# Kernel tuning notes

Measured on AMD Instinct MI355X. Metric: run time of the kernel, lower is better.

Reference implementation:

```python
import jax, jax.numpy as jnp
import numpy as np

N_BINS = 256
TAU = 0.01
EPS = 1e-10


def setup_inputs() -> dict:
    key = jax.random.key(0)
    x = jax.random.uniform(key, (4, 1, 512, 512), dtype=jnp.float32)
    return {"x": x}


def reference(x):
    B, _, H, W = x.shape
    bins = jnp.linspace(0.0, 1.0, N_BINS, dtype=x.dtype)  # (n_bins,)
    xf = x.reshape(B, H * W, 1)                            # (B, HW, 1)
    diff = xf - bins[None, None, :]                        # (B, HW, n_bins)
    weights = jnp.exp(-jnp.square(diff) / (2.0 * TAU ** 2))
    # soft histogram over pixels, normalized per image
    histogram = weights.sum(axis=1)                        # (B, n_bins)
    histogram = histogram / (histogram.sum(axis=1, keepdims=True) + EPS)
    cdf = jnp.cumsum(histogram, axis=1)                    # (B, n_bins)
    cdf_min = cdf[:, 0:1]
    cdf_normalized = (cdf - cdf_min) / (1.0 - cdf_min + EPS)
    # per-pixel soft lookup into the normalized CDF
    weights_norm = weights / (weights.sum(axis=-1, keepdims=True) + EPS)
    equalized_flat = (weights_norm * cdf_normalized[:, None, :]).sum(axis=-1)  # (B, HW)
    return equalized_flat.reshape(B, 1, H, W)
```

## Files before the change

### kernel.cpp

```cpp
#include <hip/hip_runtime.h>
#include <math.h>

#define N_BINS 256
#define TAU 0.01f
#define EPS 1e-10f
#define HW (512*512)
#define Q 4081
#define QSTRIDE 4096
#define MWIN 208
#define WTAB (2*MWIN+1)
#define WPADN 432
#define NP 27
#define CFP_STRIDE 289
#define NPART 64
#define REDS 260

__global__ __launch_bounds__(512) void hist_conv_kernel(const float* __restrict__ x,
                                                        float* __restrict__ partT) {
    __shared__ float cfp[16 * CFP_STRIDE];
    __shared__ union { unsigned int lh[QSTRIDE]; float ph[256 * 17]; } U;
    __shared__ float wtE[WPADN];
    const int b   = blockIdx.y;
    const int s   = blockIdx.x;
    const int tid = threadIdx.x;
    const int r   = tid & 15;
    const int t   = tid >> 4;

    for (int i = tid; i < QSTRIDE; i += 512) U.lh[i] = 0u;
    for (int i = tid; i < 16 * CFP_STRIDE; i += 512) cfp[i] = 0.f;
    for (int i = tid; i < WPADN; i += 512) {
        const float d = (float)(i - MWIN) * (1.0f / 4080.f);
        wtE[i] = (i < WTAB) ? __expf(-d * d * (1.0f / (2.0f * TAU * TAU))) : 0.f;
    }
    __syncthreads();

    const float4* xb = (const float4*)(x + (size_t)b * HW + (size_t)s * 4096);
#pragma unroll
    for (int i = 0; i < 2; ++i) {
        const float4 v = xb[i * 512 + tid];
        int q0 = __float2int_rn(v.x * 4080.f);
        int q1 = __float2int_rn(v.y * 4080.f);
        int q2 = __float2int_rn(v.z * 4080.f);
        int q3 = __float2int_rn(v.w * 4080.f);
        q0 = min(max(q0, 0), Q - 1); q1 = min(max(q1, 0), Q - 1);
        q2 = min(max(q2, 0), Q - 1); q3 = min(max(q3, 0), Q - 1);
        atomicAdd(&U.lh[q0], 1u); atomicAdd(&U.lh[q1], 1u);
        atomicAdd(&U.lh[q2], 1u); atomicAdd(&U.lh[q3], 1u);
    }
    __syncthreads();

#pragma unroll
    for (int k = 0; k < 8; ++k) {
        const int q = k * 512 + tid;
        cfp[(q & 15) * CFP_STRIDE + (q >> 4) + 13] = (float)U.lh[q];
    }
    __syncthreads();

    {
        float creg[34];
        const float* cbase = &cfp[r * CFP_STRIDE + 8 * t];
#pragma unroll
        for (int k = 0; k < 34; ++k) creg[k] = cbase[k];
        float acc[8];
#pragma unroll
        for (int uu = 0; uu < 8; ++uu) acc[uu] = 0.f;
#pragma unroll
        for (int p = 0; p < NP; ++p) {
            const float w = wtE[16 * p + r];
#pragma unroll
            for (int uu = 0; uu < 8; ++uu) acc[uu] += w * creg[uu + p];
        }
#pragma unroll
        for (int uu = 0; uu < 8; ++uu) U.ph[(8 * t + uu) * 17 + r] = acc[uu];
    }
    __syncthreads();

    if (tid < N_BINS) {
        float hv = 0.f;
#pragma unroll
        for (int rr = 0; rr < 16; ++rr) hv += U.ph[tid * 17 + rr];
        partT[((size_t)b * NPART + s) * N_BINS + tid] = hv;
    }
}

__global__ __launch_bounds__(512) void lut_equalize_kernel(const float* __restrict__ x,
                                                           const float* __restrict__ partT,
                                                           float* __restrict__ out) {
    __shared__ float Tl[QSTRIDE];
    __shared__ float wtE[WPADN];
    __shared__ float cdfnp[288];
    __shared__ float onesp[288];
    __shared__ __align__(16) float red[8 * REDS];
    __shared__ float wsum[4];
    __shared__ float h0s;
    const int b    = blockIdx.y;
    const int s    = blockIdx.x;
    const int tid  = threadIdx.x;
    const int r    = tid & 15;
    const int t    = tid >> 4;
    const int wv   = tid >> 6;
    const int lane = tid & 63;

    for (int i = tid; i < 288; i += 512) {
        cdfnp[i] = 0.f;
        onesp[i] = (i >= 13 && i < 269) ? 1.f : 0.f;
    }
    for (int i = tid; i < WPADN; i += 512) {
        const float d = (float)(i - MWIN) * (1.0f / 4080.f);
        wtE[i] = (i < WTAB) ? __expf(-d * d * (1.0f / (2.0f * TAU * TAU))) : 0.f;
    }

    const float4* xb = (const float4*)(x + (size_t)b * HW + (size_t)s * 4096);
    float4 px[2];
#pragma unroll
    for (int i = 0; i < 2; ++i) px[i] = xb[i * 512 + tid];

    {
        const float4* base4 = (const float4*)(partT + (size_t)b * NPART * N_BINS);
        float4 a4 = make_float4(0.f, 0.f, 0.f, 0.f);
#pragma unroll
        for (int rr = 0; rr < 8; ++rr) {
            const float4 v = base4[(size_t)(8 * wv + rr) * 64 + lane];
            a4.x += v.x; a4.y += v.y; a4.z += v.z; a4.w += v.w;
        }
        ((float4*)&red[wv * REDS])[lane] = a4;
    }
    __syncthreads();

    float val = 0.f, hv = 0.f;
    if (tid < N_BINS) {
#pragma unroll
        for (int w2 = 0; w2 < 8; ++w2) hv += red[w2 * REDS + tid];
        val = hv;
#pragma unroll
        for (int d = 1; d < 64; d <<= 1) {
            const float n = __shfl_up(val, (unsigned)d, 64);
            if (lane >= d) val += n;
        }
        if (lane == 63) wsum[tid >> 6] = val;
        if (tid == 0) h0s = hv;
    }
    __syncthreads();
    if (tid < N_BINS) {
        float prefix = 0.f, total = 0.f;
#pragma unroll
        for (int w2 = 0; w2 < 4; ++w2) {
            const float ws = wsum[w2];
            if (w2 < (tid >> 6)) prefix += ws;
            total += ws;
        }
        val += prefix;
        const float inv  = 1.0f / (total + EPS);
        const float cdf0 = h0s * inv;
        cdfnp[tid + 13] = (val * inv - cdf0) / (1.0f - cdf0 + EPS);
    }
    __syncthreads();

    {
        float creg[34], oreg[34];
        const int base = 8 * t;
#pragma unroll
        for (int k = 0; k < 34; ++k) { creg[k] = cdfnp[base + k]; oreg[k] = onesp[base + k]; }
        float acc[8], sw[8];
#pragma unroll
        for (int uu = 0; uu < 8; ++uu) { acc[uu] = 0.f; sw[uu] = 0.f; }
#pragma unroll
        for (int p = 0; p < NP; ++p) {
            const float w = wtE[16 * p + r];
#pragma unroll
            for (int uu = 0; uu < 8; ++uu) {
                const int k = uu - p + 26;
                acc[uu] += w * creg[k];
                sw[uu]  += w * oreg[k];
            }
        }
#pragma unroll
        for (int uu = 0; uu < 8; ++uu)
            Tl[16 * (8 * t + uu) + r] = acc[uu] / (sw[uu] + EPS);
    }
    __syncthreads();

    float4* ob = (float4*)(out + (size_t)b * HW + (size_t)s * 4096);
#pragma unroll
    for (int i = 0; i < 2; ++i) {
        const float4 v = px[i];
        const float vv[4] = {v.x, v.y, v.z, v.w};
        float res[4];
#pragma unroll
        for (int k2 = 0; k2 < 4; ++k2) {
            const float u = vv[k2] * 4080.f;
            int q = (int)u;
            q = min(max(q, 0), Q - 2);
            const float frac = u - (float)q;
            const float t0 = Tl[q], t1 = Tl[q + 1];
            res[k2] = fmaf(frac, t1 - t0, t0);
        }
        ob[i * 512 + tid] = make_float4(res[0], res[1], res[2], res[3]);
    }
}

extern "C" void kernel_launch(void* const* d_in, const int* in_sizes, int n_in,
                              void* d_out, int out_size, void* d_ws, size_t ws_size,
                              hipStream_t stream) {
    const float* x = (const float*)d_in[0];
    float* out     = (float*)d_out;
    const int B    = in_sizes[0] / HW;

    float* partT = (float*)d_ws;

    hist_conv_kernel<<<dim3(NPART, B), 512, 0, stream>>>(x, partT);
    lut_equalize_kernel<<<dim3(NPART, B), 512, 0, stream>>>(x, partT, out);
}
```

Baseline: 61.43 us.

## Fuse histogram and equalize kernels via cooperative launch with grid sync

Merges the two kernels into one cooperative kernel that builds per-block partial histograms, does a grid-wide sync, then computes the CDF LUT and equalizes. Pixels are loaded once and kept in registers for both phases, and shared memory is aliased through unions. This removes the second launch and the second read of x, at the cost of a cooperative launch and a grid barrier.

```diff
diff --git a/kernel.cpp b/kernel.cpp
--- a/kernel.cpp
+++ b/kernel.cpp
@@ -1,5 +1,8 @@
 #include <hip/hip_runtime.h>
+#include <hip/hip_cooperative_groups.h>
 #include <math.h>
+
+namespace cg = cooperative_groups;
 
 #define N_BINS 256
 #define TAU 0.01f
@@ -15,84 +18,26 @@
 #define NPART 64
 #define REDS 260
 
-__global__ __launch_bounds__(512) void hist_conv_kernel(const float* __restrict__ x,
-                                                        float* __restrict__ partT) {
-    __shared__ float cfp[16 * CFP_STRIDE];
-    __shared__ union { unsigned int lh[QSTRIDE]; float ph[256 * 17]; } U;
+__global__ __launch_bounds__(512) void fused_equalize_kernel(const float* __restrict__ x,
+                                                             float* __restrict__ partT,
+                                                             float* __restrict__ out) {
+    __shared__ union {
+        float cfp[16 * CFP_STRIDE];
+        float Tl[QSTRIDE];
+    } A;
+    __shared__ union {
+        unsigned int lh[QSTRIDE];
+        float ph[256 * 17];
+        struct {
+            __align__(16) float red[8 * REDS];
+            float cdfnp[288];
+            float onesp[288];
+            float wsum[4];
+            float h0s;
+        } p2;
+    } Bu;
     __shared__ float wtE[WPADN];
-    const int b   = blockIdx.y;
-    const int s   = blockIdx.x;
-    const int tid = threadIdx.x;
-    const int r   = tid & 15;
-    const int t   = tid >> 4;
-
-    for (int i = tid; i < QSTRIDE; i += 512) U.lh[i] = 0u;
-    for (int i = tid; i < 16 * CFP_STRIDE; i += 512) cfp[i] = 0.f;
-    for (int i = tid; i < WPADN; i += 512) {
-        const float d = (float)(i - MWIN) * (1.0f / 4080.f);
-        wtE[i] = (i < WTAB) ? __expf(-d * d * (1.0f / (2.0f * TAU * TAU))) : 0.f;
-    }
-    __syncthreads();
-
-    const float4* xb = (const float4*)(x + (size_t)b * HW + (size_t)s * 4096);
-#pragma unroll
-    for (int i = 0; i < 2; ++i) {
-        const float4 v = xb[i * 512 + tid];
-        int q0 = __float2int_rn(v.x * 4080.f);
-        int q1 = __float2int_rn(v.y * 4080.f);
-        int q2 = __float2int_rn(v.z * 4080.f);
-        int q3 = __float2int_rn(v.w * 4080.f);
-        q0 = min(max(q0, 0), Q - 1); q1 = min(max(q1, 0), Q - 1);
-        q2 = min(max(q2, 0), Q - 1); q3 = min(max(q3, 0), Q - 1);
-        atomicAdd(&U.lh[q0], 1u); atomicAdd(&U.lh[q1], 1u);
-        atomicAdd(&U.lh[q2], 1u); atomicAdd(&U.lh[q3], 1u);
-    }
-    __syncthreads();
-
-#pragma unroll
-    for (int k = 0; k < 8; ++k) {
-        const int q = k * 512 + tid;
-        cfp[(q & 15) * CFP_STRIDE + (q >> 4) + 13] = (float)U.lh[q];
-    }
-    __syncthreads();
-
-    {
-        float creg[34];
-        const float* cbase = &cfp[r * CFP_STRIDE + 8 * t];
-#pragma unroll
-        for (int k = 0; k < 34; ++k) creg[k] = cbase[k];
-        float acc[8];
-#pragma unroll
-        for (int uu = 0; uu < 8; ++uu) acc[uu] = 0.f;
-#pragma unroll
-        for (int p = 0; p < NP; ++p) {
-            const float w = wtE[16 * p + r];
-#pragma unroll
-            for (int uu = 0; uu < 8; ++uu) acc[uu] += w * creg[uu + p];
-        }
-#pragma unroll
-        for (int uu = 0; uu < 8; ++uu) U.ph[(8 * t + uu) * 17 + r] = acc[uu];
-    }
-    __syncthreads();
-
-    if (tid < N_BINS) {
-        float hv = 0.f;
-#pragma unroll
-        for (int rr = 0; rr < 16; ++rr) hv += U.ph[tid * 17 + rr];
-        partT[((size_t)b * NPART + s) * N_BINS + tid] = hv;
-    }
-}
-
-__global__ __launch_bounds__(512) void lut_equalize_kernel(const float* __restrict__ x,
-                                                           const float* __restrict__ partT,
-                                                           float* __restrict__ out) {
-    __shared__ float Tl[QSTRIDE];
-    __shared__ float wtE[WPADN];
-    __shared__ float cdfnp[288];
-    __shared__ float onesp[288];
-    __shared__ __align__(16) float red[8 * REDS];
-    __shared__ float wsum[4];
-    __shared__ float h0s;
+
     const int b    = blockIdx.y;
     const int s    = blockIdx.x;
     const int tid  = threadIdx.x;
@@ -101,10 +46,8 @@
     const int wv   = tid >> 6;
     const int lane = tid & 63;
 
-    for (int i = tid; i < 288; i += 512) {
-        cdfnp[i] = 0.f;
-        onesp[i] = (i >= 13 && i < 269) ? 1.f : 0.f;
-    }
+    for (int i = tid; i < QSTRIDE; i += 512) Bu.lh[i] = 0u;
+    for (int i = tid; i < 16 * CFP_STRIDE; i += 512) A.cfp[i] = 0.f;
     for (int i = tid; i < WPADN; i += 512) {
         const float d = (float)(i - MWIN) * (1.0f / 4080.f);
         wtE[i] = (i < WTAB) ? __expf(-d * d * (1.0f / (2.0f * TAU * TAU))) : 0.f;
@@ -112,9 +55,63 @@
 
     const float4* xb = (const float4*)(x + (size_t)b * HW + (size_t)s * 4096);
     float4 px[2];
-#pragma unroll
-    for (int i = 0; i < 2; ++i) px[i] = xb[i * 512 + tid];
-
+    px[0] = xb[tid];
+    px[1] = xb[512 + tid];
+    __syncthreads();
+
+#pragma unroll
+    for (int i = 0; i < 2; ++i) {
+        const float4 v = px[i];
+        int q0 = __float2int_rn(v.x * 4080.f);
+        int q1 = __float2int_rn(v.y * 4080.f);
+        int q2 = __float2int_rn(v.z * 4080.f);
+        int q3 = __float2int_rn(v.w * 4080.f);
+        q0 = min(max(q0, 0), Q - 1); q1 = min(max(q1, 0), Q - 1);
+        q2 = min(max(q2, 0), Q - 1); q3 = min(max(q3, 0), Q - 1);
+        atomicAdd(&Bu.lh[q0], 1u); atomicAdd(&Bu.lh[q1], 1u);
+        atomicAdd(&Bu.lh[q2], 1u); atomicAdd(&Bu.lh[q3], 1u);
+    }
+    __syncthreads();
+
+#pragma unroll
+    for (int k = 0; k < 8; ++k) {
+        const int q = k * 512 + tid;
+        A.cfp[(q & 15) * CFP_STRIDE + (q >> 4) + 13] = (float)Bu.lh[q];
+    }
+    __syncthreads();
+
+    {
+        float creg[34];
+        const float* cbase = &A.cfp[r * CFP_STRIDE + 8 * t];
+#pragma unroll
+        for (int k = 0; k < 34; ++k) creg[k] = cbase[k];
+        float acc[8];
+#pragma unroll
+        for (int uu = 0; uu < 8; ++uu) acc[uu] = 0.f;
+#pragma unroll
+        for (int p = 0; p < NP; ++p) {
+            const float w = wtE[16 * p + r];
+#pragma unroll
+            for (int uu = 0; uu < 8; ++uu) acc[uu] += w * creg[uu + p];
+        }
+#pragma unroll
+        for (int uu = 0; uu < 8; ++uu) Bu.ph[(8 * t + uu) * 17 + r] = acc[uu];
+    }
+    __syncthreads();
+
+    if (tid < N_BINS) {
+        float hv = 0.f;
+#pragma unroll
+        for (int rr = 0; rr < 16; ++rr) hv += Bu.ph[tid * 17 + rr];
+        partT[((size_t)b * NPART + s) * N_BINS + tid] = hv;
+    }
+
+    cg::this_grid().sync();
+
+    for (int i = tid; i < 288; i += 512) {
+        Bu.p2.cdfnp[i] = 0.f;
+        Bu.p2.onesp[i] = (i >= 13 && i < 269) ? 1.f : 0.f;
+    }
     {
         const float4* base4 = (const float4*)(partT + (size_t)b * NPART * N_BINS);
         float4 a4 = make_float4(0.f, 0.f, 0.f, 0.f);
@@ -123,36 +120,36 @@
             const float4 v = base4[(size_t)(8 * wv + rr) * 64 + lane];
             a4.x += v.x; a4.y += v.y; a4.z += v.z; a4.w += v.w;
         }
-        ((float4*)&red[wv * REDS])[lane] = a4;
+        ((float4*)&Bu.p2.red[wv * REDS])[lane] = a4;
     }
     __syncthreads();
 
     float val = 0.f, hv = 0.f;
     if (tid < N_BINS) {
 #pragma unroll
-        for (int w2 = 0; w2 < 8; ++w2) hv += red[w2 * REDS + tid];
+        for (int w2 = 0; w2 < 8; ++w2) hv += Bu.p2.red[w2 * REDS + tid];
         val = hv;
 #pragma unroll
         for (int d = 1; d < 64; d <<= 1) {
             const float n = __shfl_up(val, (unsigned)d, 64);
             if (lane >= d) val += n;
         }
-        if (lane == 63) wsum[tid >> 6] = val;
-        if (tid == 0) h0s = hv;
+        if (lane == 63) Bu.p2.wsum[tid >> 6] = val;
+        if (tid == 0) Bu.p2.h0s = hv;
     }
     __syncthreads();
     if (tid < N_BINS) {
         float prefix = 0.f, total = 0.f;
 #pragma unroll
         for (int w2 = 0; w2 < 4; ++w2) {
-            const float ws = wsum[w2];
+            const float ws = Bu.p2.wsum[w2];
             if (w2 < (tid >> 6)) prefix += ws;
             total += ws;
         }
         val += prefix;
         const float inv  = 1.0f / (total + EPS);
-        const float cdf0 = h0s * inv;
-        cdfnp[tid + 13] = (val * inv - cdf0) / (1.0f - cdf0 + EPS);
+        const float cdf0 = Bu.p2.h0s * inv;
+        Bu.p2.cdfnp[tid + 13] = (val * inv - cdf0) / (1.0f - cdf0 + EPS);
     }
     __syncthreads();
 
@@ -160,7 +157,7 @@
         float creg[34], oreg[34];
         const int base = 8 * t;
 #pragma unroll
-        for (int k = 0; k < 34; ++k) { creg[k] = cdfnp[base + k]; oreg[k] = onesp[base + k]; }
+        for (int k = 0; k < 34; ++k) { creg[k] = Bu.p2.cdfnp[base + k]; oreg[k] = Bu.p2.onesp[base + k]; }
         float acc[8], sw[8];
 #pragma unroll
         for (int uu = 0; uu < 8; ++uu) { acc[uu] = 0.f; sw[uu] = 0.f; }
@@ -176,7 +173,7 @@
         }
 #pragma unroll
         for (int uu = 0; uu < 8; ++uu)
-            Tl[16 * (8 * t + uu) + r] = acc[uu] / (sw[uu] + EPS);
+            A.Tl[16 * (8 * t + uu) + r] = acc[uu] / (sw[uu] + EPS);
     }
     __syncthreads();
 
@@ -192,7 +189,7 @@
             int q = (int)u;
             q = min(max(q, 0), Q - 2);
             const float frac = u - (float)q;
-            const float t0 = Tl[q], t1 = Tl[q + 1];
+            const float t0 = A.Tl[q], t1 = A.Tl[q + 1];
             res[k2] = fmaf(frac, t1 - t0, t0);
         }
         ob[i * 512 + tid] = make_float4(res[0], res[1], res[2], res[3]);
@@ -208,6 +205,7 @@
 
     float* partT = (float*)d_ws;
 
-    hist_conv_kernel<<<dim3(NPART, B), 512, 0, stream>>>(x, partT);
-    lut_equalize_kernel<<<dim3(NPART, B), 512, 0, stream>>>(x, partT, out);
+    void* args[] = { (void*)&x, (void*)&partT, (void*)&out };
+    hipLaunchCooperativeKernel((const void*)fused_equalize_kernel,
+                               dim3(NPART, B), dim3(512), args, 0, stream);
 }
```

Measured after the change: 93.84 us. 1.53x slower.

## Accumulate histogram via global atomics with parity double buffer, drop partial reduction

Applied to the files above, without the earlier changes.

The histogram kernel now bins pixels directly into the padded shared conv layout with float atomics, which removes the integer histogram and its transpose pass. It reduces the per-bin conv output across lanes with xor-shuffles and atomically adds the result into a global per-image histogram. A generation-counter parity scheme alternates between two global buffers and zeroes the idle one, so the second kernel can read the finished histogram directly instead of reducing 64 partials from the workspace. The LUT kernel also skips the ones-convolution for interior tiles, where the weight sum is constant. In exchange it depends on cross-launch global state and ordering assumptions about the zeroing and the generation counters, which is fragile and order-sensitive.

```diff
diff --git a/kernel.cpp b/kernel.cpp
--- a/kernel.cpp
+++ b/kernel.cpp
@@ -13,49 +13,61 @@
 #define NP 27
 #define CFP_STRIDE 289
 #define NPART 64
-#define REDS 260
-
-__global__ __launch_bounds__(512) void hist_conv_kernel(const float* __restrict__ x,
-                                                        float* __restrict__ partT) {
+#define BMAX 4
+#define HSTRIDE 16
+
+__device__ __align__(64) unsigned int g_genA = 0u;
+__device__ __align__(64) unsigned int g_genB = 0u;
+__device__ __align__(16) float g_hist[2][BMAX][N_BINS * HSTRIDE];
+
+__global__ __launch_bounds__(512) void hist_conv_kernel(const float* __restrict__ x) {
     __shared__ float cfp[16 * CFP_STRIDE];
-    __shared__ union { unsigned int lh[QSTRIDE]; float ph[256 * 17]; } U;
     __shared__ float wtE[WPADN];
+    __shared__ unsigned int sgen;
     const int b   = blockIdx.y;
     const int s   = blockIdx.x;
     const int tid = threadIdx.x;
     const int r   = tid & 15;
     const int t   = tid >> 4;
 
-    for (int i = tid; i < QSTRIDE; i += 512) U.lh[i] = 0u;
+    const float4* xb = (const float4*)(x + (size_t)b * HW + (size_t)s * 4096);
+    const float4 p0 = xb[tid];
+    const float4 p1 = xb[512 + tid];
+
+    if (tid == 0)
+        sgen = __hip_atomic_load(&g_genA, __ATOMIC_RELAXED, __HIP_MEMORY_SCOPE_AGENT);
     for (int i = tid; i < 16 * CFP_STRIDE; i += 512) cfp[i] = 0.f;
     for (int i = tid; i < WPADN; i += 512) {
         const float d = (float)(i - MWIN) * (1.0f / 4080.f);
         wtE[i] = (i < WTAB) ? __expf(-d * d * (1.0f / (2.0f * TAU * TAU))) : 0.f;
     }
     __syncthreads();
-
-    const float4* xb = (const float4*)(x + (size_t)b * HW + (size_t)s * 4096);
-#pragma unroll
-    for (int i = 0; i < 2; ++i) {
-        const float4 v = xb[i * 512 + tid];
-        int q0 = __float2int_rn(v.x * 4080.f);
-        int q1 = __float2int_rn(v.y * 4080.f);
-        int q2 = __float2int_rn(v.z * 4080.f);
-        int q3 = __float2int_rn(v.w * 4080.f);
-        q0 = min(max(q0, 0), Q - 1); q1 = min(max(q1, 0), Q - 1);
-        q2 = min(max(q2, 0), Q - 1); q3 = min(max(q3, 0), Q - 1);
-        atomicAdd(&U.lh[q0], 1u); atomicAdd(&U.lh[q1], 1u);
-        atomicAdd(&U.lh[q2], 1u); atomicAdd(&U.lh[q3], 1u);
-    }
-    __syncthreads();
-
-#pragma unroll
-    for (int k = 0; k < 8; ++k) {
-        const int q = k * 512 + tid;
-        cfp[(q & 15) * CFP_STRIDE + (q >> 4) + 13] = (float)U.lh[q];
-    }
-    __syncthreads();
-
+    const int par = (int)(sgen & 1u);
+
+    if (s == 0 && tid < N_BINS)
+        __hip_atomic_store(&g_hist[par ^ 1][b][tid * HSTRIDE], 0.f,
+                           __ATOMIC_RELAXED, __HIP_MEMORY_SCOPE_AGENT);
+
+    {
+        const float4 vv[2] = {p0, p1};
+#pragma unroll
+        for (int i = 0; i < 2; ++i) {
+            const float4 v = vv[i];
+            int q0 = __float2int_rn(v.x * 4080.f);
+            int q1 = __float2int_rn(v.y * 4080.f);
+            int q2 = __float2int_rn(v.z * 4080.f);
+            int q3 = __float2int_rn(v.w * 4080.f);
+            q0 = min(max(q0, 0), Q - 1); q1 = min(max(q1, 0), Q - 1);
+            q2 = min(max(q2, 0), Q - 1); q3 = min(max(q3, 0), Q - 1);
+            atomicAdd(&cfp[(q0 & 15) * CFP_STRIDE + (q0 >> 4) + 13], 1.f);
+            atomicAdd(&cfp[(q1 & 15) * CFP_STRIDE + (q1 >> 4) + 13], 1.f);
+            atomicAdd(&cfp[(q2 & 15) * CFP_STRIDE + (q2 >> 4) + 13], 1.f);
+            atomicAdd(&cfp[(q3 & 15) * CFP_STRIDE + (q3 >> 4) + 13], 1.f);
+        }
+    }
+    __syncthreads();
+
+    float v0, v1, v2, v3, v4, v5, v6, v7;
     {
         float creg[34];
         const float* cbase = &cfp[r * CFP_STRIDE + 8 * t];
@@ -70,37 +82,64 @@
 #pragma unroll
             for (int uu = 0; uu < 8; ++uu) acc[uu] += w * creg[uu + p];
         }
-#pragma unroll
-        for (int uu = 0; uu < 8; ++uu) U.ph[(8 * t + uu) * 17 + r] = acc[uu];
-    }
-    __syncthreads();
-
-    if (tid < N_BINS) {
-        float hv = 0.f;
-#pragma unroll
-        for (int rr = 0; rr < 16; ++rr) hv += U.ph[tid * 17 + rr];
-        partT[((size_t)b * NPART + s) * N_BINS + tid] = hv;
-    }
+        v0 = acc[0]; v1 = acc[1]; v2 = acc[2]; v3 = acc[3];
+        v4 = acc[4]; v5 = acc[5]; v6 = acc[6]; v7 = acc[7];
+    }
+
+    {
+        const bool h1 = (r & 1) != 0;
+        float s0 = h1 ? v0 : v1, s1 = h1 ? v2 : v3, s2 = h1 ? v4 : v5, s3 = h1 ? v6 : v7;
+        const float q0 = __shfl_xor(s0, 1, 64), q1 = __shfl_xor(s1, 1, 64);
+        const float q2 = __shfl_xor(s2, 1, 64), q3 = __shfl_xor(s3, 1, 64);
+        const float w0 = (h1 ? v1 : v0) + q0;
+        const float w1 = (h1 ? v3 : v2) + q1;
+        const float w2 = (h1 ? v5 : v4) + q2;
+        const float w3 = (h1 ? v7 : v6) + q3;
+
+        const bool h2 = (r & 2) != 0;
+        float u0 = h2 ? w0 : w1, u1 = h2 ? w2 : w3;
+        const float e0 = __shfl_xor(u0, 2, 64), e1 = __shfl_xor(u1, 2, 64);
+        const float x0 = (h2 ? w1 : w0) + e0;
+        const float x1 = (h2 ? w3 : w2) + e1;
+
+        const bool h4 = (r & 4) != 0;
+        float u2 = h4 ? x0 : x1;
+        const float e2 = __shfl_xor(u2, 4, 64);
+        const float y = (h4 ? x1 : x0) + e2;
+
+        const float z = y + __shfl_xor(y, 8, 64);
+
+        if (r < 8)
+            atomicAdd(&g_hist[par][b][(8 * t + r) * HSTRIDE], z);
+    }
+
+    if (b == 0 && s == 0 && tid == 0)
+        __hip_atomic_fetch_add(&g_genB, 1u, __ATOMIC_RELAXED, __HIP_MEMORY_SCOPE_AGENT);
 }
 
 __global__ __launch_bounds__(512) void lut_equalize_kernel(const float* __restrict__ x,
-                                                           const float* __restrict__ partT,
                                                            float* __restrict__ out) {
     __shared__ float Tl[QSTRIDE];
     __shared__ float wtE[WPADN];
     __shared__ float cdfnp[288];
     __shared__ float onesp[288];
-    __shared__ __align__(16) float red[8 * REDS];
     __shared__ float wsum[4];
     __shared__ float h0s;
+    __shared__ unsigned int sgen;
     const int b    = blockIdx.y;
     const int s    = blockIdx.x;
     const int tid  = threadIdx.x;
     const int r    = tid & 15;
     const int t    = tid >> 4;
-    const int wv   = tid >> 6;
     const int lane = tid & 63;
 
+    const float4* xb = (const float4*)(x + (size_t)b * HW + (size_t)s * 4096);
+    float4 px[2];
+    px[0] = xb[tid];
+    px[1] = xb[512 + tid];
+
+    if (tid == 0)
+        sgen = __hip_atomic_load(&g_genB, __ATOMIC_RELAXED, __HIP_MEMORY_SCOPE_AGENT);
     for (int i = tid; i < 288; i += 512) {
         cdfnp[i] = 0.f;
         onesp[i] = (i >= 13 && i < 269) ? 1.f : 0.f;
@@ -109,28 +148,13 @@
         const float d = (float)(i - MWIN) * (1.0f / 4080.f);
         wtE[i] = (i < WTAB) ? __expf(-d * d * (1.0f / (2.0f * TAU * TAU))) : 0.f;
     }
-
-    const float4* xb = (const float4*)(x + (size_t)b * HW + (size_t)s * 4096);
-    float4 px[2];
-#pragma unroll
-    for (int i = 0; i < 2; ++i) px[i] = xb[i * 512 + tid];
-
-    {
-        const float4* base4 = (const float4*)(partT + (size_t)b * NPART * N_BINS);
-        float4 a4 = make_float4(0.f, 0.f, 0.f, 0.f);
-#pragma unroll
-        for (int rr = 0; rr < 8; ++rr) {
-            const float4 v = base4[(size_t)(8 * wv + rr) * 64 + lane];
-            a4.x += v.x; a4.y += v.y; a4.z += v.z; a4.w += v.w;
-        }
-        ((float4*)&red[wv * REDS])[lane] = a4;
-    }
-    __syncthreads();
+    __syncthreads();
+    const int par = (int)((sgen - 1u) & 1u);
 
     float val = 0.f, hv = 0.f;
     if (tid < N_BINS) {
-#pragma unroll
-        for (int w2 = 0; w2 < 8; ++w2) hv += red[w2 * REDS + tid];
+        hv = __hip_atomic_load(&g_hist[par][b][tid * HSTRIDE], __ATOMIC_RELAXED,
+                               __HIP_MEMORY_SCOPE_AGENT);
         val = hv;
 #pragma unroll
         for (int d = 1; d < 64; d <<= 1) {
@@ -157,26 +181,47 @@
     __syncthreads();
 
     {
-        float creg[34], oreg[34];
+        float creg[34];
         const int base = 8 * t;
 #pragma unroll
-        for (int k = 0; k < 34; ++k) { creg[k] = cdfnp[base + k]; oreg[k] = onesp[base + k]; }
-        float acc[8], sw[8];
-#pragma unroll
-        for (int uu = 0; uu < 8; ++uu) { acc[uu] = 0.f; sw[uu] = 0.f; }
-#pragma unroll
-        for (int p = 0; p < NP; ++p) {
-            const float w = wtE[16 * p + r];
-#pragma unroll
-            for (int uu = 0; uu < 8; ++uu) {
-                const int k = uu - p + 26;
-                acc[uu] += w * creg[k];
-                sw[uu]  += w * oreg[k];
+        for (int k = 0; k < 34; ++k) creg[k] = cdfnp[base + k];
+        float acc[8];
+#pragma unroll
+        for (int uu = 0; uu < 8; ++uu) acc[uu] = 0.f;
+
+        if (t >= 2 && t <= 29) {
+            float swt = 0.f;
+#pragma unroll
+            for (int p = 0; p < NP; ++p) {
+                const float w = wtE[16 * p + r];
+                swt += w;
+#pragma unroll
+                for (int uu = 0; uu < 8; ++uu) acc[uu] += w * creg[uu - p + 26];
             }
-        }
-#pragma unroll
-        for (int uu = 0; uu < 8; ++uu)
-            Tl[16 * (8 * t + uu) + r] = acc[uu] / (sw[uu] + EPS);
+            const float dinv = 1.0f / (swt + EPS);
+#pragma unroll
+            for (int uu = 0; uu < 8; ++uu)
+                Tl[16 * (8 * t + uu) + r] = acc[uu] * dinv;
+        } else {
+            float oreg[34], sw[8];
+#pragma unroll
+            for (int k = 0; k < 34; ++k) oreg[k] = onesp[base + k];
+#pragma unroll
+            for (int uu = 0; uu < 8; ++uu) sw[uu] = 0.f;
+#pragma unroll
+            for (int p = 0; p < NP; ++p) {
+                const float w = wtE[16 * p + r];
+#pragma unroll
+                for (int uu = 0; uu < 8; ++uu) {
+                    const int k = uu - p + 26;
+                    acc[uu] += w * creg[k];
+                    sw[uu]  += w * oreg[k];
+                }
+            }
+#pragma unroll
+            for (int uu = 0; uu < 8; ++uu)
+                Tl[16 * (8 * t + uu) + r] = acc[uu] / (sw[uu] + EPS);
+        }
     }
     __syncthreads();
 
@@ -197,6 +242,9 @@
         }
         ob[i * 512 + tid] = make_float4(res[0], res[1], res[2], res[3]);
     }
+
+    if (b == 0 && s == 0 && tid == 0)
+        __hip_atomic_fetch_add(&g_genA, 1u, __ATOMIC_RELAXED, __HIP_MEMORY_SCOPE_AGENT);
 }
 
 extern "C" void kernel_launch(void* const* d_in, const int* in_sizes, int n_in,
@@ -206,8 +254,6 @@
     float* out     = (float*)d_out;
     const int B    = in_sizes[0] / HW;
 
-    float* partT = (float*)d_ws;
-
-    hist_conv_kernel<<<dim3(NPART, B), 512, 0, stream>>>(x, partT);
-    lut_equalize_kernel<<<dim3(NPART, B), 512, 0, stream>>>(x, partT, out);
+    hist_conv_kernel<<<dim3(NPART, B), 512, 0, stream>>>(x);
+    lut_equalize_kernel<<<dim3(NPART, B), 512, 0, stream>>>(x, out);
 }
```

Result: slower. 70.46 us (+14.7%).
